# Optimization experiments

Measured on AMD Instinct MI355X. Metric: run time of the kernel, lower is better.

Reference implementation:

```python
import jax, jax.numpy as jnp
from jax import lax
import numpy as np

H = 8          # n_heads
K = 4          # n_points == KNN k (hardcoded k=4 in original)
NN = 4         # neighbors per sampling point
D_MODEL = 256


def setup_inputs() -> dict:
    key = jax.random.key(0)
    ks = jax.random.split(key, 16)
    b, n_q, n_kv, d = 2, 1024, 2048, D_MODEL
    query = jax.random.normal(ks[0], (b, n_q, d), dtype=jnp.float32)
    query_pos = jax.random.uniform(ks[1], (b, n_q, 2), dtype=jnp.float32)
    key_value = jax.random.normal(ks[2], (b, n_kv, d), dtype=jnp.float32)
    kv_pos = jax.random.uniform(ks[3], (b, n_kv, 2), dtype=jnp.float32)
    # sampling_offsets linear: small weights + rotated-grid bias (as in _reset_parameters, scaled
    # so sampling locations stay near the unit square of kv positions)
    W_off = 0.001 * jax.random.normal(ks[4], (d, H * K * 2), dtype=jnp.float32)
    thetas = np.arange(H, dtype=np.float32) * (2.0 * np.pi / H)
    grid = np.stack([np.cos(thetas), np.sin(thetas)], -1)          # [H,2]
    grid = grid / np.abs(grid).max(-1, keepdims=True)
    grid = np.repeat(grid[:, None, :], K, axis=1)                  # [H,K,2]
    grid = grid * (np.arange(1, K + 1, dtype=np.float32)[None, :, None])
    b_off = jnp.asarray(0.05 * grid.reshape(-1), dtype=jnp.float32)
    W_attn = 0.02 * jax.random.normal(ks[5], (d, H * K), dtype=jnp.float32)
    b_attn = jnp.zeros((H * K,), dtype=jnp.float32)
    xav = (6.0 / (d + d)) ** 0.5
    W_v = jax.random.uniform(ks[6], (d, d), minval=-xav, maxval=xav, dtype=jnp.float32)
    b_v = jnp.zeros((d,), dtype=jnp.float32)
    W_out = jax.random.uniform(ks[7], (d, d), minval=-xav, maxval=xav, dtype=jnp.float32)
    b_out = jnp.zeros((d,), dtype=jnp.float32)
    shepard_power = jnp.asarray(1.0, dtype=jnp.float32)
    return {"query": query, "query_pos": query_pos, "key_value": key_value, "kv_pos": kv_pos,
            "W_off": W_off, "b_off": b_off, "W_attn": W_attn, "b_attn": b_attn,
            "W_v": W_v, "b_v": b_v, "W_out": W_out, "b_out": b_out,
            "shepard_power": shepard_power}


def _deform_attn(query, query_pos, key_value, kv_pos,
                 W_off, b_off, W_attn, b_attn, W_v, b_v, W_out, b_out, shepard_power):
    b, n_q, c = query.shape
    n_kv = key_value.shape[1]
    c_ = c // H
    # projections
    off = (query @ W_off + b_off).reshape(b, n_q, H, K, 2)
    attn = jax.nn.softmax((query @ W_attn + b_attn).reshape(b, n_q, H, K), axis=-1)
    values = (key_value @ W_v + b_v).reshape(b, n_kv, H, c_)
    values = values.transpose(0, 2, 1, 3).reshape(b * H, n_kv, c_)
    # sampling locations [b*H, n_q*K, 2]
    loc = (query_pos[:, :, None, None, :] + off).transpose(0, 2, 1, 3, 4)
    loc = loc.reshape(b * H, n_q * K, 2)
    kvp = jnp.broadcast_to(kv_pos[:, None], (b, H, n_kv, 2)).reshape(b * H, n_kv, 2)
    # brute-force KNN (k=4) on squared distances via GEMM expansion
    d2 = ((loc * loc).sum(-1)[:, :, None] + (kvp * kvp).sum(-1)[:, None, :]
          - 2.0 * jnp.einsum('bqd,bkd->bqk', loc, kvp))           # [bH, nqK, n_kv]
    _, nb_idx = lax.top_k(-d2, NN)                                 # [bH, nqK, 4]
    bidx = jnp.arange(b * H)[:, None, None]
    nb_pos = kvp[bidx, nb_idx]                                     # [bH, nqK, 4, 2]
    dist = jnp.linalg.norm(nb_pos - loc[:, :, None, :], axis=-1) + 1e-6
    power = jax.nn.relu(shepard_power) + 1e-6
    nn_w = jax.nn.softmax(-power * dist, axis=-1)                  # Shepard weights over 4 nbrs
    nn_w = nn_w.reshape(b * H, n_q, K, NN)
    idx = nb_idx.reshape(b * H, n_q, K, NN)
    attn_r = attn.transpose(0, 2, 1, 3).reshape(b * H, n_q, K)
    vg = values[jnp.arange(b * H)[:, None, None, None], idx]       # [bH, n_q, K, 4, c_]
    out = jnp.einsum('bqp,bqpn,bqpnc->bqc', attn_r, nn_w, vg)      # [bH, n_q, c_]
    out = out.reshape(b, H, n_q, c_).transpose(0, 2, 1, 3).reshape(b, n_q, c)
    return out @ W_out + b_out


def reference(query, query_pos, key_value, kv_pos,
              W_off, b_off, W_attn, b_attn, W_v, b_v, W_out, b_out, shepard_power):
    return _deform_attn(query, query_pos, key_value, kv_pos,
                        W_off, b_off, W_attn, b_attn, W_v, b_v, W_out, b_out, shepard_power)
```

## Files before the change

### kernel.cpp

```cpp
#include <hip/hip_runtime.h>
#include <hip/hip_bf16.h>
#include <math.h>

#define H 8
#define K 4
#define NN 4
#define D 256
#define NQ 1024
#define NKV 2048
#define BATCH 2
#define CH 32
#define GC 16
#define CELLH 0.0625f

#define OFF_LOC   0u
#define OFF_ATTN  524288u
#define OFF_VWS   786432u
#define OFF_HEAD  4980736u
#define OFF_PTS   7077888u
#define OFF_CST   7143424u
#define WS_NEED   7147520u

typedef unsigned short ushortb;

__device__ __forceinline__ float bf2f(ushortb u) {
    return __uint_as_float((unsigned)u << 16);
}
__device__ __forceinline__ ushortb f2bf(float f) {
    __hip_bfloat16 h = __float2bfloat16(f);
    return *(ushortb*)&h;
}

__device__ __forceinline__ void lexins(float t, int n,
                                       float& d0, float& d1, float& d2, float& d3,
                                       int& i0, int& i1, int& i2, int& i3) {
    bool c0 = (t < d0) || (t == d0 && n < i0);
    bool c1 = (t < d1) || (t == d1 && n < i1);
    bool c2 = (t < d2) || (t == d2 && n < i2);
    bool c3 = (t < d3) || (t == d3 && n < i3);
    d3 = c3 ? (c2 ? d2 : t) : d3;   i3 = c3 ? (c2 ? i2 : n) : i3;
    d2 = c2 ? (c1 ? d1 : t) : d2;   i2 = c2 ? (c1 ? i1 : n) : i2;
    d1 = c1 ? (c0 ? d0 : t) : d1;   i1 = c1 ? (c0 ? i0 : n) : i1;
    d0 = c0 ? t : d0;               i0 = c0 ? n : i0;
}

__device__ __forceinline__ void lexins_d(float t, int n,
                                         float& d0, float& d1, float& d2, float& d3,
                                         int& i0, int& i1, int& i2, int& i3) {
    bool nd = !((n == i0) | (n == i1) | (n == i2) | (n == i3));
    bool c0 = nd && ((t < d0) || (t == d0 && n < i0));
    bool c1 = nd && ((t < d1) || (t == d1 && n < i1));
    bool c2 = nd && ((t < d2) || (t == d2 && n < i2));
    bool c3 = nd && ((t < d3) || (t == d3 && n < i3));
    d3 = c3 ? (c2 ? d2 : t) : d3;   i3 = c3 ? (c2 ? i2 : n) : i3;
    d2 = c2 ? (c1 ? d1 : t) : d2;   i2 = c2 ? (c1 ? i1 : n) : i2;
    d1 = c1 ? (c0 ? d0 : t) : d1;   i1 = c1 ? (c0 ? i0 : n) : i1;
    d0 = c0 ? t : d0;               i0 = c0 ? n : i0;
}

__device__ __forceinline__ void bins4(float t, int n,
                                      float& d0, float& d1, float& d2, float& d3,
                                      int& i0, int& i1, int& i2, int& i3) {
    bool c0 = t < d0, c1 = t < d1, c2 = t < d2, c3 = t < d3;
    d3 = c3 ? (c2 ? d2 : t) : d3;   i3 = c3 ? (c2 ? i2 : n) : i3;
    d2 = c2 ? (c1 ? d1 : t) : d2;   i2 = c2 ? (c1 ? i1 : n) : i2;
    d1 = c1 ? (c0 ? d0 : t) : d1;   i1 = c1 ? (c0 ? i0 : n) : i1;
    d0 = c0 ? t : d0;               i0 = c0 ? n : i0;
}

__global__ void k_offattn(const float* __restrict__ q, const float* __restrict__ qpos,
                          const float* __restrict__ Woff, const float* __restrict__ boff,
                          const float* __restrict__ Wattn, const float* __restrict__ battn,
                          float* __restrict__ loc, float* __restrict__ attnw) {
    #pragma clang fp contract(off)
    int row = blockIdx.x;
    int b = row >> 10, qi = row & (NQ - 1);
    __shared__ float qs[D];
    for (int d = threadIdx.x; d < D; d += blockDim.x) qs[d] = q[(size_t)row * D + d];
    __syncthreads();
    int j = threadIdx.x;
    if (j < 64) {
        float acc = 0.0f;
        for (int d = 0; d < D; ++d) acc = fmaf(qs[d], Woff[d * 64 + j], acc);
        float off = acc + boff[j];
        int xy = j & 1;
        int hk = j >> 1;
        int h = hk >> 2, k = hk & 3;
        float L = qpos[(size_t)row * 2 + xy] + off;
        int g = ((b * H + h) * NQ + qi) * K + k;
        loc[(size_t)g * 2 + xy] = L;
    } else if (j < 96) {
        int j2 = j - 64;
        float acc = 0.0f;
        for (int d = 0; d < D; ++d) acc = fmaf(qs[d], Wattn[d * 32 + j2], acc);
        acc += battn[j2];
        float m = acc;
        m = fmaxf(m, __shfl_xor(m, 1));
        m = fmaxf(m, __shfl_xor(m, 2));
        float e = expf(acc - m);
        float s = e;
        s += __shfl_xor(s, 1);
        s += __shfl_xor(s, 2);
        float w = e / s;
        int h = j2 >> 2, k = j2 & 3;
        attnw[((b * H + h) * NQ + qi) * K + k] = w;
    }
}

__global__ void k_values(const float* __restrict__ kv, const float* __restrict__ Wv,
                         const float* __restrict__ bv, ushortb* __restrict__ vwsb) {
    int r0 = blockIdx.x * 4;
    __shared__ float ks[4][D];
    for (int t = threadIdx.x; t < 4 * D; t += 256) ks[t >> 8][t & 255] = kv[(size_t)r0 * D + t];
    __syncthreads();
    int c = threadIdx.x;
    float a0 = 0.f, a1 = 0.f, a2 = 0.f, a3 = 0.f;
    for (int d = 0; d < D; ++d) {
        float w = Wv[d * D + c];
        a0 = fmaf(ks[0][d], w, a0); a1 = fmaf(ks[1][d], w, a1);
        a2 = fmaf(ks[2][d], w, a2); a3 = fmaf(ks[3][d], w, a3);
    }
    float bias = bv[c];
    a0 += bias; a1 += bias; a2 += bias; a3 += bias;
    int h = c >> 5, cc = c & 31;
    float va[4] = {a0, a1, a2, a3};
    for (int r = 0; r < 4; ++r) {
        int row = r0 + r;
        int b = row >> 11, n = row & (NKV - 1);
        vwsb[(((size_t)(b * H + h) * NKV) + n) * CH + cc] = f2bf(va[r]);
    }
}

__global__ void k_bin(const float* __restrict__ kvpos, float4* __restrict__ pts4,
                      int* __restrict__ cellStart) {
    #pragma clang fp contract(off)
    int b = blockIdx.x;
    int tid = threadIdx.x;
    __shared__ int cnt[GC * GC];
    __shared__ int ofs[GC * GC + 1];
    __shared__ int cur[GC * GC];
    if (tid < GC * GC) cnt[tid] = 0;
    __syncthreads();
    for (int n = tid; n < NKV; n += 256) {
        float x = kvpos[(size_t)(b * NKV + n) * 2 + 0];
        float y = kvpos[(size_t)(b * NKV + n) * 2 + 1];
        int ix = min(GC - 1, max(0, (int)floorf(x * (float)GC)));
        int iy = min(GC - 1, max(0, (int)floorf(y * (float)GC)));
        atomicAdd(&cnt[iy * GC + ix], 1);
    }
    __syncthreads();
    if (tid == 0) {
        int s = 0;
        for (int c = 0; c < GC * GC; ++c) { ofs[c] = s; s += cnt[c]; }
        ofs[GC * GC] = s;
    }
    __syncthreads();
    for (int t = tid; t < GC * GC + 1; t += 256) cellStart[b * 257 + t] = ofs[t];
    if (tid < GC * GC) cur[tid] = ofs[tid];
    __syncthreads();
    for (int n = tid; n < NKV; n += 256) {
        float x = kvpos[(size_t)(b * NKV + n) * 2 + 0];
        float y = kvpos[(size_t)(b * NKV + n) * 2 + 1];
        int ix = min(GC - 1, max(0, (int)floorf(x * (float)GC)));
        int iy = min(GC - 1, max(0, (int)floorf(y * (float)GC)));
        int pos = atomicAdd(&cur[iy * GC + ix], 1);
        pts4[(size_t)b * NKV + pos] = make_float4(-2.0f * x, -2.0f * y, x * x + y * y, (float)n);
    }
}

__global__ void k_knn_grid2(const float* __restrict__ kvpos, const float* __restrict__ loc,
                            const float* __restrict__ attnw, const ushortb* __restrict__ vwsb,
                            const float* __restrict__ sp,
                            const float4* __restrict__ pts4, const int* __restrict__ cellStart,
                            float* __restrict__ head) {
    #pragma clang fp contract(off)
    int lane = threadIdx.x;
    int s = lane & 7;
    int g = blockIdx.x * 32 + (lane >> 3);
    int b = g >> 15;
    int bh = g >> 12;

    __shared__ int cst[GC * GC + 1];
    for (int i = threadIdx.x; i < GC * GC + 1; i += 256) cst[i] = cellStart[b * 257 + i];
    __syncthreads();

    const float4* gp = pts4 + (size_t)b * NKV;
    float2 L = ((const float2*)loc)[g];
    float lx = L.x, ly = L.y;
    float sl = lx * lx + ly * ly;

    int ix = min(GC - 1, max(0, (int)floorf(lx * (float)GC)));
    int iy = min(GC - 1, max(0, (int)floorf(ly * (float)GC)));

    float d0 = 1e30f, d1 = 1e30f, d2 = 1e30f, d3 = 1e30f;
    int i0 = 0x7FFFFFFF, i1 = 0x7FFFFFFF, i2 = 0x7FFFFFFF, i3 = 0x7FFFFFFF;

#define INS1(P) { float tt = (sl + (P).z) + fmaf(ly, (P).y, lx * (P).x);      \
                  lexins(tt, (int)(P).w, d0, d1, d2, d3, i0, i1, i2, i3); }

    {
        int bx0 = max(ix - 1, 0), bx1 = min(ix + 1, GC - 1);
        int by0 = max(iy - 1, 0), by1 = min(iy + 1, GC - 1);
        int a0 = cst[by0 * GC + bx0];
        int l0 = cst[by0 * GC + bx1 + 1] - a0;
        int a1 = 0, l1 = 0, a2 = 0, l2 = 0;
        if (by0 + 1 <= by1) { a1 = cst[(by0 + 1) * GC + bx0]; l1 = cst[(by0 + 1) * GC + bx1 + 1] - a1; }
        if (by0 + 2 <= by1) { a2 = cst[(by0 + 2) * GC + bx0]; l2 = cst[(by0 + 2) * GC + bx1 + 1] - a2; }
        int l01 = l0 + l1;
        int m = l01 + l2;
        int f = s;
        for (; f + 24 < m; f += 32) {
            int f0 = f, f1 = f + 8, f2 = f + 16, f3 = f + 24;
            int j0 = f0 < l0 ? a0 + f0 : (f0 < l01 ? a1 + (f0 - l0) : a2 + (f0 - l01));
            int j1 = f1 < l0 ? a0 + f1 : (f1 < l01 ? a1 + (f1 - l0) : a2 + (f1 - l01));
            int j2 = f2 < l0 ? a0 + f2 : (f2 < l01 ? a1 + (f2 - l0) : a2 + (f2 - l01));
            int j3 = f3 < l0 ? a0 + f3 : (f3 < l01 ? a1 + (f3 - l0) : a2 + (f3 - l01));
            float4 p0 = gp[j0], p1 = gp[j1], p2 = gp[j2], p3 = gp[j3];
            INS1(p0); INS1(p1); INS1(p2); INS1(p3);
        }
        for (; f < m; f += 8) {
            int j = f < l0 ? a0 + f : (f < l01 ? a1 + (f - l0) : a2 + (f - l01));
            float4 p = gp[j];
            INS1(p);
        }
    }

#define MERGE_P(M) {                                                           \
        float e0 = __shfl_xor(d0, M), e1 = __shfl_xor(d1, M);                  \
        float e2 = __shfl_xor(d2, M), e3 = __shfl_xor(d3, M);                  \
        int j0 = __shfl_xor(i0, M), j1 = __shfl_xor(i1, M);                    \
        int j2 = __shfl_xor(i2, M), j3 = __shfl_xor(i3, M);                    \
        lexins(e0, j0, d0, d1, d2, d3, i0, i1, i2, i3);                        \
        lexins(e1, j1, d0, d1, d2, d3, i0, i1, i2, i3);                        \
        lexins(e2, j2, d0, d1, d2, d3, i0, i1, i2, i3);                        \
        lexins(e3, j3, d0, d1, d2, d3, i0, i1, i2, i3);                        \
    }
#define MERGE_D(M) {                                                           \
        float e0 = __shfl_xor(d0, M), e1 = __shfl_xor(d1, M);                  \
        float e2 = __shfl_xor(d2, M), e3 = __shfl_xor(d3, M);                  \
        int j0 = __shfl_xor(i0, M), j1 = __shfl_xor(i1, M);                    \
        int j2 = __shfl_xor(i2, M), j3 = __shfl_xor(i3, M);                    \
        lexins_d(e0, j0, d0, d1, d2, d3, i0, i1, i2, i3);                      \
        lexins_d(e1, j1, d0, d1, d2, d3, i0, i1, i2, i3);                      \
        lexins_d(e2, j2, d0, d1, d2, d3, i0, i1, i2, i3);                      \
        lexins_d(e3, j3, d0, d1, d2, d3, i0, i1, i2, i3);                      \
    }

    MERGE_P(1);
    MERGE_P(2);
    MERGE_P(4);

    auto done_at = [&](int r) -> bool {
        int bx0 = ix - r, bx1 = ix + r, by0 = iy - r, by1 = iy + r;
        float bound = 1e30f;
        if (bx0 > 0)      bound = fminf(bound, lx - (float)bx0 * CELLH);
        if (bx1 < GC - 1) bound = fminf(bound, (float)(bx1 + 1) * CELLH - lx);
        if (by0 > 0)      bound = fminf(bound, ly - (float)by0 * CELLH);
        if (by1 < GC - 1) bound = fminf(bound, (float)(by1 + 1) * CELLH - ly);
        bool covered = (bx0 <= 0 && bx1 >= GC - 1 && by0 <= 0 && by1 >= GC - 1);
        return covered || (d3 < bound * bound - 1e-5f);
    };

#define SCAN_RANGE_S(JLO, JHI)                                       \
    for (int j = (JLO) + s; j < (JHI); j += 8) {                     \
        float4 p = gp[j];                                            \
        INS1(p);                                                     \
    }

    int r = 1;
    bool need = !done_at(1);
    while (__any(need)) {
        ++r;
        if (need) {
            int ry0 = iy - r, ry1 = iy + r;
            int rx0 = ix - r, rx1 = ix + r;
            int ca = max(rx0, 0), cb = min(rx1, GC - 1);
            if (ry0 >= 0)      { int base = ry0 * GC; SCAN_RANGE_S(cst[base + ca], cst[base + cb + 1]); }
            if (ry1 <= GC - 1) { int base = ry1 * GC; SCAN_RANGE_S(cst[base + ca], cst[base + cb + 1]); }
            int ya = max(ry0 + 1, 0), yb = min(ry1 - 1, GC - 1);
            if (rx0 >= 0)      for (int cy = ya; cy <= yb; ++cy) { int c = cy * GC + rx0; SCAN_RANGE_S(cst[c], cst[c + 1]); }
            if (rx1 <= GC - 1) for (int cy = ya; cy <= yb; ++cy) { int c = cy * GC + rx1; SCAN_RANGE_S(cst[c], cst[c + 1]); }
            MERGE_D(1);
            MERGE_D(2);
            MERGE_D(4);
            need = !done_at(r);
        }
    }
#undef SCAN_RANGE_S
#undef MERGE_P
#undef MERGE_D
#undef INS1

    int bb = bh >> 3, h = bh & 7;
    int qi = (g >> 2) & (NQ - 1);
    float power = fmaxf(sp[0], 0.0f) + 1e-6f;
    int idx[4] = {i0, i1, i2, i3};
    float z[4];
    #pragma unroll
    for (int u = 0; u < 4; ++u) {
        float kx = kvpos[(size_t)(bb * NKV + idx[u]) * 2 + 0];
        float ky = kvpos[(size_t)(bb * NKV + idx[u]) * 2 + 1];
        float dx = kx - lx;
        float dy = ky - ly;
        float dist = sqrtf(dx * dx + dy * dy) + 1e-6f;
        z[u] = -power * dist;
    }
    float m = fmaxf(fmaxf(z[0], z[1]), fmaxf(z[2], z[3]));
    float e0 = expf(z[0] - m), e1 = expf(z[1] - m), e2 = expf(z[2] - m), e3 = expf(z[3] - m);
    float esum = e0 + e1 + e2 + e3;
    float w0 = e0 / esum, w1 = e1 / esum, w2 = e2 / esum, w3 = e3 / esum;

    const ushort4* vp0 = (const ushort4*)(vwsb + ((size_t)bh * NKV + i0) * CH);
    const ushort4* vp1 = (const ushort4*)(vwsb + ((size_t)bh * NKV + i1) * CH);
    const ushort4* vp2 = (const ushort4*)(vwsb + ((size_t)bh * NKV + i2) * CH);
    const ushort4* vp3 = (const ushort4*)(vwsb + ((size_t)bh * NKV + i3) * CH);
    float a = attnw[g];
    float4* hp = (float4*)(head + ((size_t)(bb * NQ + qi)) * D + h * CH);
    {
        ushort4 u0 = vp0[s], u1 = vp1[s], u2 = vp2[s], u3 = vp3[s];
        float4 rr;
        rr.x = a * (w0 * bf2f(u0.x) + w1 * bf2f(u1.x) + w2 * bf2f(u2.x) + w3 * bf2f(u3.x));
        rr.y = a * (w0 * bf2f(u0.y) + w1 * bf2f(u1.y) + w2 * bf2f(u2.y) + w3 * bf2f(u3.y));
        rr.z = a * (w0 * bf2f(u0.z) + w1 * bf2f(u1.z) + w2 * bf2f(u2.z) + w3 * bf2f(u3.z));
        rr.w = a * (w0 * bf2f(u0.w) + w1 * bf2f(u1.w) + w2 * bf2f(u2.w) + w3 * bf2f(u3.w));
        rr.x += __shfl_xor(rr.x, 8); rr.x += __shfl_xor(rr.x, 16);
        rr.y += __shfl_xor(rr.y, 8); rr.y += __shfl_xor(rr.y, 16);
        rr.z += __shfl_xor(rr.z, 8); rr.z += __shfl_xor(rr.z, 16);
        rr.w += __shfl_xor(rr.w, 8); rr.w += __shfl_xor(rr.w, 16);
        if (((lane >> 3) & 3) == 0) hp[s] = rr;
    }
}

__global__ void k_knn_fused(const float* __restrict__ kvpos, const float* __restrict__ loc,
                            const float* __restrict__ attnw, const ushortb* __restrict__ vwsb,
                            const float* __restrict__ sp, float* __restrict__ head) {
    #pragma clang fp contract(off)
    int g = blockIdx.x * 256 + threadIdx.x;
    int bh = g >> 12;
    int b = bh >> 3;
    __shared__ float sx[NKV];
    __shared__ float sy[NKV];
    __shared__ float sz[NKV];
    for (int n = threadIdx.x; n < NKV; n += 256) {
        float x = kvpos[(size_t)(b * NKV + n) * 2 + 0];
        float y = kvpos[(size_t)(b * NKV + n) * 2 + 1];
        sx[n] = -2.0f * x;
        sy[n] = -2.0f * y;
        sz[n] = x * x + y * y;
    }
    __syncthreads();
    float2 L = ((const float2*)loc)[g];
    float lx = L.x, ly = L.y;
    float sl = lx * lx + ly * ly;
    const float4* x4 = (const float4*)sx;
    const float4* y4 = (const float4*)sy;
    const float4* z4 = (const float4*)sz;
    float d0 = 1e30f, d1 = 1e30f, d2 = 1e30f, d3 = 1e30f;
    int i0 = 0, i1 = 0, i2 = 0, i3 = 0;
    for (int n = 0; n < NKV; n += 4) {
        int v = n >> 2;
        float4 xA = x4[v], yA = y4[v], zA = z4[v];
        float t0 = (sl + zA.x) + fmaf(ly, yA.x, lx * xA.x);
        float t1 = (sl + zA.y) + fmaf(ly, yA.y, lx * xA.y);
        float t2 = (sl + zA.z) + fmaf(ly, yA.z, lx * xA.z);
        float t3 = (sl + zA.w) + fmaf(ly, yA.w, lx * xA.w);
        bins4(t0, n + 0, d0, d1, d2, d3, i0, i1, i2, i3);
        bins4(t1, n + 1, d0, d1, d2, d3, i0, i1, i2, i3);
        bins4(t2, n + 2, d0, d1, d2, d3, i0, i1, i2, i3);
        bins4(t3, n + 3, d0, d1, d2, d3, i0, i1, i2, i3);
    }
    float power = fmaxf(sp[0], 0.0f) + 1e-6f;
    int h = bh & 7;
    int qi = (g >> 2) & (NQ - 1);
    int k = g & 3;
    int idx[4] = {i0, i1, i2, i3};
    float z[4];
    #pragma unroll
    for (int u = 0; u < 4; ++u) {
        float kx = kvpos[(size_t)(b * NKV + idx[u]) * 2 + 0];
        float ky = kvpos[(size_t)(b * NKV + idx[u]) * 2 + 1];
        float dx = kx - lx;
        float dy = ky - ly;
        float dist = sqrtf(dx * dx + dy * dy) + 1e-6f;
        z[u] = -power * dist;
    }
    float m = fmaxf(fmaxf(z[0], z[1]), fmaxf(z[2], z[3]));
    float e0 = expf(z[0] - m), e1 = expf(z[1] - m), e2 = expf(z[2] - m), e3 = expf(z[3] - m);
    float esum = e0 + e1 + e2 + e3;
    float w0 = e0 / esum, w1 = e1 / esum, w2 = e2 / esum, w3 = e3 / esum;
    const ushort4* vp0 = (const ushort4*)(vwsb + ((size_t)bh * NKV + i0) * CH);
    const ushort4* vp1 = (const ushort4*)(vwsb + ((size_t)bh * NKV + i1) * CH);
    const ushort4* vp2 = (const ushort4*)(vwsb + ((size_t)bh * NKV + i2) * CH);
    const ushort4* vp3 = (const ushort4*)(vwsb + ((size_t)bh * NKV + i3) * CH);
    float a = attnw[g];
    float4 acc[8];
    #pragma unroll
    for (int t = 0; t < 8; ++t) {
        ushort4 u0 = vp0[t], u1 = vp1[t], u2 = vp2[t], u3 = vp3[t];
        float4 r;
        r.x = a * (w0 * bf2f(u0.x) + w1 * bf2f(u1.x) + w2 * bf2f(u2.x) + w3 * bf2f(u3.x));
        r.y = a * (w0 * bf2f(u0.y) + w1 * bf2f(u1.y) + w2 * bf2f(u2.y) + w3 * bf2f(u3.y));
        r.z = a * (w0 * bf2f(u0.z) + w1 * bf2f(u1.z) + w2 * bf2f(u2.z) + w3 * bf2f(u3.z));
        r.w = a * (w0 * bf2f(u0.w) + w1 * bf2f(u1.w) + w2 * bf2f(u2.w) + w3 * bf2f(u3.w));
        r.x += __shfl_xor(r.x, 1); r.x += __shfl_xor(r.x, 2);
        r.y += __shfl_xor(r.y, 1); r.y += __shfl_xor(r.y, 2);
        r.z += __shfl_xor(r.z, 1); r.z += __shfl_xor(r.z, 2);
        r.w += __shfl_xor(r.w, 1); r.w += __shfl_xor(r.w, 2);
        acc[t] = r;
    }
    float4* hp = (float4*)(head + ((size_t)(b * NQ + qi)) * D + h * CH);
    hp[k * 2]     = acc[k * 2];
    hp[k * 2 + 1] = acc[k * 2 + 1];
}

__global__ void k_out(const float* __restrict__ head, const float* __restrict__ Wout,
                      const float* __restrict__ bout, float* __restrict__ out) {
    int r0 = blockIdx.x * 4;
    __shared__ float hs[4][D];
    for (int t = threadIdx.x; t < 4 * D; t += 256) hs[t >> 8][t & 255] = head[(size_t)r0 * D + t];
    __syncthreads();
    int c = threadIdx.x;
    float a0 = 0.f, a1 = 0.f, a2 = 0.f, a3 = 0.f;
    for (int d = 0; d < D; ++d) {
        float w = Wout[d * D + c];
        a0 = fmaf(hs[0][d], w, a0); a1 = fmaf(hs[1][d], w, a1);
        a2 = fmaf(hs[2][d], w, a2); a3 = fmaf(hs[3][d], w, a3);
    }
    float bias = bout[c];
    out[(size_t)(r0 + 0) * D + c] = a0 + bias;
    out[(size_t)(r0 + 1) * D + c] = a1 + bias;
    out[(size_t)(r0 + 2) * D + c] = a2 + bias;
    out[(size_t)(r0 + 3) * D + c] = a3 + bias;
}

extern "C" void kernel_launch(void* const* d_in, const int* in_sizes, int n_in,
                              void* d_out, int out_size, void* d_ws, size_t ws_size,
                              hipStream_t stream) {
    (void)in_sizes; (void)n_in; (void)out_size;
    const float* q     = (const float*)d_in[0];
    const float* qpos  = (const float*)d_in[1];
    const float* kv    = (const float*)d_in[2];
    const float* kvp   = (const float*)d_in[3];
    const float* Woff  = (const float*)d_in[4];
    const float* boff  = (const float*)d_in[5];
    const float* Wattn = (const float*)d_in[6];
    const float* battn = (const float*)d_in[7];
    const float* Wv    = (const float*)d_in[8];
    const float* bv    = (const float*)d_in[9];
    const float* Wout  = (const float*)d_in[10];
    const float* bout  = (const float*)d_in[11];
    const float* sp    = (const float*)d_in[12];
    float* out = (float*)d_out;

    char* ws = (char*)d_ws;
    float* loc      = (float*)(ws + OFF_LOC);
    float* attnw    = (float*)(ws + OFF_ATTN);
    ushortb* vwsb   = (ushortb*)(ws + OFF_VWS);
    float* head     = (float*)(ws + OFF_HEAD);
    float4* pts4    = (float4*)(ws + OFF_PTS);
    int* cellStart  = (int*)(ws + OFF_CST);

    hipLaunchKernelGGL(k_offattn, dim3(BATCH * NQ), dim3(128), 0, stream,
                       q, qpos, Woff, boff, Wattn, battn, loc, attnw);
    hipLaunchKernelGGL(k_values, dim3(BATCH * NKV / 4), dim3(256), 0, stream,
                       kv, Wv, bv, vwsb);
    if (ws_size >= (size_t)WS_NEED) {
        hipLaunchKernelGGL(k_bin, dim3(BATCH), dim3(256), 0, stream,
                           kvp, pts4, cellStart);
        hipLaunchKernelGGL(k_knn_grid2, dim3(BATCH * H * NQ * K / 32), dim3(256), 0, stream,
                           kvp, loc, attnw, vwsb, sp, pts4, cellStart, head);
    } else {
        hipLaunchKernelGGL(k_knn_fused, dim3(BATCH * H * NQ * K / 256), dim3(256), 0, stream,
                           kvp, loc, attnw, vwsb, sp, head);
    }
    hipLaunchKernelGGL(k_out, dim3(BATCH * NQ / 4), dim3(256), 0, stream,
                       head, Wout, bout, out);
}
```

Before: 114.7 us.

## Merge offset/attn projection, value projection and binning into one front kernel

```diff
diff --git a/kernel.cpp b/kernel.cpp
--- a/kernel.cpp
+++ b/kernel.cpp
@@ -68,103 +68,109 @@
     d0 = c0 ? t : d0;               i0 = c0 ? n : i0;
 }
 
-__global__ void k_offattn(const float* __restrict__ q, const float* __restrict__ qpos,
-                          const float* __restrict__ Woff, const float* __restrict__ boff,
-                          const float* __restrict__ Wattn, const float* __restrict__ battn,
-                          float* __restrict__ loc, float* __restrict__ attnw) {
+__global__ void k_front(const float* __restrict__ q, const float* __restrict__ qpos,
+                        const float* __restrict__ Woff, const float* __restrict__ boff,
+                        const float* __restrict__ Wattn, const float* __restrict__ battn,
+                        const float* __restrict__ kv, const float* __restrict__ Wv,
+                        const float* __restrict__ bv, const float* __restrict__ kvpos,
+                        float* __restrict__ loc, float* __restrict__ attnw,
+                        ushortb* __restrict__ vwsb,
+                        float4* __restrict__ pts4, int* __restrict__ cellStart) {
     #pragma clang fp contract(off)
-    int row = blockIdx.x;
-    int b = row >> 10, qi = row & (NQ - 1);
-    __shared__ float qs[D];
-    for (int d = threadIdx.x; d < D; d += blockDim.x) qs[d] = q[(size_t)row * D + d];
-    __syncthreads();
-    int j = threadIdx.x;
-    if (j < 64) {
-        float acc = 0.0f;
-        for (int d = 0; d < D; ++d) acc = fmaf(qs[d], Woff[d * 64 + j], acc);
-        float off = acc + boff[j];
-        int xy = j & 1;
-        int hk = j >> 1;
-        int h = hk >> 2, k = hk & 3;
-        float L = qpos[(size_t)row * 2 + xy] + off;
-        int g = ((b * H + h) * NQ + qi) * K + k;
-        loc[(size_t)g * 2 + xy] = L;
-    } else if (j < 96) {
-        int j2 = j - 64;
-        float acc = 0.0f;
-        for (int d = 0; d < D; ++d) acc = fmaf(qs[d], Wattn[d * 32 + j2], acc);
-        acc += battn[j2];
-        float m = acc;
-        m = fmaxf(m, __shfl_xor(m, 1));
-        m = fmaxf(m, __shfl_xor(m, 2));
-        float e = expf(acc - m);
-        float s = e;
-        s += __shfl_xor(s, 1);
-        s += __shfl_xor(s, 2);
-        float w = e / s;
-        int h = j2 >> 2, k = j2 & 3;
-        attnw[((b * H + h) * NQ + qi) * K + k] = w;
-    }
-}
-
-__global__ void k_values(const float* __restrict__ kv, const float* __restrict__ Wv,
-                         const float* __restrict__ bv, ushortb* __restrict__ vwsb) {
-    int r0 = blockIdx.x * 4;
-    __shared__ float ks[4][D];
-    for (int t = threadIdx.x; t < 4 * D; t += 256) ks[t >> 8][t & 255] = kv[(size_t)r0 * D + t];
-    __syncthreads();
-    int c = threadIdx.x;
-    float a0 = 0.f, a1 = 0.f, a2 = 0.f, a3 = 0.f;
-    for (int d = 0; d < D; ++d) {
-        float w = Wv[d * D + c];
-        a0 = fmaf(ks[0][d], w, a0); a1 = fmaf(ks[1][d], w, a1);
-        a2 = fmaf(ks[2][d], w, a2); a3 = fmaf(ks[3][d], w, a3);
-    }
-    float bias = bv[c];
-    a0 += bias; a1 += bias; a2 += bias; a3 += bias;
-    int h = c >> 5, cc = c & 31;
-    float va[4] = {a0, a1, a2, a3};
-    for (int r = 0; r < 4; ++r) {
-        int row = r0 + r;
-        int b = row >> 11, n = row & (NKV - 1);
-        vwsb[(((size_t)(b * H + h) * NKV) + n) * CH + cc] = f2bf(va[r]);
-    }
-}
-
-__global__ void k_bin(const float* __restrict__ kvpos, float4* __restrict__ pts4,
-                      int* __restrict__ cellStart) {
-    #pragma clang fp contract(off)
-    int b = blockIdx.x;
-    int tid = threadIdx.x;
-    __shared__ int cnt[GC * GC];
-    __shared__ int ofs[GC * GC + 1];
-    __shared__ int cur[GC * GC];
-    if (tid < GC * GC) cnt[tid] = 0;
-    __syncthreads();
-    for (int n = tid; n < NKV; n += 256) {
-        float x = kvpos[(size_t)(b * NKV + n) * 2 + 0];
-        float y = kvpos[(size_t)(b * NKV + n) * 2 + 1];
-        int ix = min(GC - 1, max(0, (int)floorf(x * (float)GC)));
-        int iy = min(GC - 1, max(0, (int)floorf(y * (float)GC)));
-        atomicAdd(&cnt[iy * GC + ix], 1);
-    }
-    __syncthreads();
-    if (tid == 0) {
-        int s = 0;
-        for (int c = 0; c < GC * GC; ++c) { ofs[c] = s; s += cnt[c]; }
-        ofs[GC * GC] = s;
-    }
-    __syncthreads();
-    for (int t = tid; t < GC * GC + 1; t += 256) cellStart[b * 257 + t] = ofs[t];
-    if (tid < GC * GC) cur[tid] = ofs[tid];
-    __syncthreads();
-    for (int n = tid; n < NKV; n += 256) {
-        float x = kvpos[(size_t)(b * NKV + n) * 2 + 0];
-        float y = kvpos[(size_t)(b * NKV + n) * 2 + 1];
-        int ix = min(GC - 1, max(0, (int)floorf(x * (float)GC)));
-        int iy = min(GC - 1, max(0, (int)floorf(y * (float)GC)));
-        int pos = atomicAdd(&cur[iy * GC + ix], 1);
-        pts4[(size_t)b * NKV + pos] = make_float4(-2.0f * x, -2.0f * y, x * x + y * y, (float)n);
+    if (blockIdx.x < (BATCH * NQ) / 2) {
+        int r0 = blockIdx.x * 2;
+        __shared__ float qs2[2][D];
+        for (int t = threadIdx.x; t < 2 * D; t += 256) qs2[t >> 8][t & 255] = q[(size_t)r0 * D + t];
+        __syncthreads();
+        int half = threadIdx.x >> 7;
+        int j = threadIdx.x & 127;
+        int row = r0 + half;
+        int b = row >> 10, qi = row & (NQ - 1);
+        const float* qs = qs2[half];
+        if (j < 64) {
+            float acc = 0.0f;
+            for (int d = 0; d < D; ++d) acc = fmaf(qs[d], Woff[d * 64 + j], acc);
+            float off = acc + boff[j];
+            int xy = j & 1;
+            int hk = j >> 1;
+            int h = hk >> 2, k = hk & 3;
+            float L = qpos[(size_t)row * 2 + xy] + off;
+            int g = ((b * H + h) * NQ + qi) * K + k;
+            loc[(size_t)g * 2 + xy] = L;
+        } else if (j < 96) {
+            int j2 = j - 64;
+            float acc = 0.0f;
+            for (int d = 0; d < D; ++d) acc = fmaf(qs[d], Wattn[d * 32 + j2], acc);
+            acc += battn[j2];
+            float m = acc;
+            m = fmaxf(m, __shfl_xor(m, 1));
+            m = fmaxf(m, __shfl_xor(m, 2));
+            float e = expf(acc - m);
+            float s = e;
+            s += __shfl_xor(s, 1);
+            s += __shfl_xor(s, 2);
+            float w = e / s;
+            int h = j2 >> 2, k = j2 & 3;
+            attnw[((b * H + h) * NQ + qi) * K + k] = w;
+        }
+        return;
+    }
+    if (blockIdx.x < (BATCH * NQ) / 2 + BATCH * NKV / 4) {
+        int r0 = (blockIdx.x - (BATCH * NQ) / 2) * 4;
+        __shared__ float ks[4][D];
+        for (int t = threadIdx.x; t < 4 * D; t += 256) ks[t >> 8][t & 255] = kv[(size_t)r0 * D + t];
+        __syncthreads();
+        int c = threadIdx.x;
+        float a0 = 0.f, a1 = 0.f, a2 = 0.f, a3 = 0.f;
+        for (int d = 0; d < D; ++d) {
+            float w = Wv[d * D + c];
+            a0 = fmaf(ks[0][d], w, a0); a1 = fmaf(ks[1][d], w, a1);
+            a2 = fmaf(ks[2][d], w, a2); a3 = fmaf(ks[3][d], w, a3);
+        }
+        float bias = bv[c];
+        a0 += bias; a1 += bias; a2 += bias; a3 += bias;
+        int h = c >> 5, cc = c & 31;
+        float va[4] = {a0, a1, a2, a3};
+        for (int r = 0; r < 4; ++r) {
+            int row = r0 + r;
+            int b = row >> 11, n = row & (NKV - 1);
+            vwsb[(((size_t)(b * H + h) * NKV) + n) * CH + cc] = f2bf(va[r]);
+        }
+        return;
+    }
+    {
+        int b = blockIdx.x - ((BATCH * NQ) / 2 + BATCH * NKV / 4);
+        int tid = threadIdx.x;
+        __shared__ int cnt[GC * GC];
+        __shared__ int ofs[GC * GC + 1];
+        __shared__ int cur[GC * GC];
+        if (tid < GC * GC) cnt[tid] = 0;
+        __syncthreads();
+        for (int n = tid; n < NKV; n += 256) {
+            float x = kvpos[(size_t)(b * NKV + n) * 2 + 0];
+            float y = kvpos[(size_t)(b * NKV + n) * 2 + 1];
+            int ix = min(GC - 1, max(0, (int)floorf(x * (float)GC)));
+            int iy = min(GC - 1, max(0, (int)floorf(y * (float)GC)));
+            atomicAdd(&cnt[iy * GC + ix], 1);
+        }
+        __syncthreads();
+        if (tid == 0) {
+            int s = 0;
+            for (int c = 0; c < GC * GC; ++c) { ofs[c] = s; s += cnt[c]; }
+            ofs[GC * GC] = s;
+        }
+        __syncthreads();
+        for (int t = tid; t < GC * GC + 1; t += 256) cellStart[b * 257 + t] = ofs[t];
+        if (tid < GC * GC) cur[tid] = ofs[tid];
+        __syncthreads();
+        for (int n = tid; n < NKV; n += 256) {
+            float x = kvpos[(size_t)(b * NKV + n) * 2 + 0];
+            float y = kvpos[(size_t)(b * NKV + n) * 2 + 1];
+            int ix = min(GC - 1, max(0, (int)floorf(x * (float)GC)));
+            int iy = min(GC - 1, max(0, (int)floorf(y * (float)GC)));
+            int pos = atomicAdd(&cur[iy * GC + ix], 1);
+            pts4[(size_t)b * NKV + pos] = make_float4(-2.0f * x, -2.0f * y, x * x + y * y, (float)n);
+        }
     }
 }
 
@@ -460,13 +466,12 @@
     float4* pts4    = (float4*)(ws + OFF_PTS);
     int* cellStart  = (int*)(ws + OFF_CST);
 
-    hipLaunchKernelGGL(k_offattn, dim3(BATCH * NQ), dim3(128), 0, stream,
-                       q, qpos, Woff, boff, Wattn, battn, loc, attnw);
-    hipLaunchKernelGGL(k_values, dim3(BATCH * NKV / 4), dim3(256), 0, stream,
-                       kv, Wv, bv, vwsb);
-    if (ws_size >= (size_t)WS_NEED) {
-        hipLaunchKernelGGL(k_bin, dim3(BATCH), dim3(256), 0, stream,
-                           kvp, pts4, cellStart);
+    bool grid_ok = ws_size >= (size_t)WS_NEED;
+    int nfront = (BATCH * NQ) / 2 + BATCH * NKV / 4 + (grid_ok ? BATCH : 0);
+    hipLaunchKernelGGL(k_front, dim3(nfront), dim3(256), 0, stream,
+                       q, qpos, Woff, boff, Wattn, battn, kv, Wv, bv, kvp,
+                       loc, attnw, vwsb, pts4, cellStart);
+    if (grid_ok) {
         hipLaunchKernelGGL(k_knn_grid2, dim3(BATCH * H * NQ * K / 32), dim3(256), 0, stream,
                            kvp, loc, attnw, vwsb, sp, pts4, cellStart, head);
     } else {
```

Measured after the change: 103.2 us, median of 2. -10.0%, faster.
